# Kernel optimization log

Measured on AMD Instinct MI355X. Metric: run time of the kernel, lower is better.

The kernel has to match this reference:

```python
import jax, jax.numpy as jnp
import numpy as np

T = 2048        # flattened tokens (one prefill sequence)
HID = 2048      # hidden_size
NH = 32         # query heads
NKV = 4         # kv heads
HD = 128        # head_dim
THETA = 1000000.0
EPS = 1e-6


def setup_inputs() -> dict:
    key = jax.random.key(0)
    k0, k1, k2 = jax.random.split(key, 3)
    return {
        "positions": jnp.arange(T, dtype=jnp.int32),
        "hidden_states": jax.random.normal(k0, (T, HID), dtype=jnp.float32),
        "w_qkv": jax.random.normal(k1, ((NH + 2 * NKV) * HD, HID), dtype=jnp.float32) * 0.02,
        "w_o": jax.random.normal(k2, (HID, NH * HD), dtype=jnp.float32) * 0.02,
        "q_norm_w": jnp.ones((HD,), dtype=jnp.float32),
        "k_norm_w": jnp.ones((HD,), dtype=jnp.float32),
    }


def _rmsnorm(x, w):
    # per-head RMSNorm over last dim (head_dim), fp32 math
    var = jnp.mean(x * x, axis=-1, keepdims=True)
    return x * jax.lax.rsqrt(var + EPS) * w


def _rope(x, positions):
    # NeoX-style rotary embedding over full head_dim
    d = x.shape[-1]
    inv_freq = 1.0 / (THETA ** (jnp.arange(0, d, 2, dtype=jnp.float32) / d))  # [d/2]
    ang = positions.astype(jnp.float32)[:, None] * inv_freq                   # [T, d/2]
    cos = jnp.cos(ang)[:, None, :]  # [T,1,d/2]
    sin = jnp.sin(ang)[:, None, :]
    x1, x2 = jnp.split(x, 2, axis=-1)
    return jnp.concatenate([x1 * cos - x2 * sin, x2 * cos + x1 * sin], axis=-1)


def reference(positions, hidden_states, w_qkv, w_o, q_norm_w, k_norm_w):
    # fused QKV projection (no bias)
    qkv = hidden_states @ w_qkv.T                       # [T, (NH+2*NKV)*HD]
    q, k, v = jnp.split(qkv, [NH * HD, (NH + NKV) * HD], axis=-1)
    q = _rmsnorm(q.reshape(T, NH, HD), q_norm_w)        # [T,NH,HD]
    k = _rmsnorm(k.reshape(T, NKV, HD), k_norm_w)       # [T,NKV,HD]
    v = v.reshape(T, NKV, HD)
    q = _rope(q, positions)
    k = _rope(k, positions)
    # GQA: expand kv heads to query heads
    g = NH // NKV
    k = jnp.repeat(k, g, axis=1)                        # [T,NH,HD]
    v = jnp.repeat(v, g, axis=1)
    scale = HD ** -0.5
    scores = jnp.einsum('qhd,khd->hqk', q, k) * scale   # [NH,T,T]
    causal = jnp.tril(jnp.ones((T, T), dtype=bool))
    scores = jnp.where(causal[None, :, :], scores, jnp.finfo(scores.dtype).min)
    attn = jax.nn.softmax(scores, axis=-1)
    o = jnp.einsum('hqk,khd->qhd', attn, v).reshape(T, NH * HD)
    return o @ w_o.T                                    # [T,HID]
```

## Files before the change

### kernel.cpp

```cpp
#include <hip/hip_runtime.h>
#include <math.h>

#define T 2048
#define HID 2048
#define NH 32
#define NKV 4
#define HD 128
#define QKV_DIM 5120
#define OD 4096
#define C2LOG 0.12751743f
#define MFIX 6.0f

typedef _Float16 half8 __attribute__((ext_vector_type(8)));
typedef _Float16 half4v __attribute__((ext_vector_type(4)));
typedef float floatx4 __attribute__((ext_vector_type(4)));

#define GLD16(gp, lp) __builtin_amdgcn_global_load_lds( \
    (const __attribute__((address_space(1))) void*)(gp), \
    (__attribute__((address_space(3))) void*)(lp), 16, 0, 0)

__global__ __launch_bounds__(256)
void cvt_all(const float* __restrict__ h, const float* __restrict__ wq,
             const float* __restrict__ wo, _Float16* __restrict__ out) {
    size_t i = ((size_t)blockIdx.x * 256 + threadIdx.x) * 4;
    const float* src;
    size_t off;
    if (i < (size_t)T * HID)                        { src = h;  off = i; }
    else if (i < (size_t)T * HID + (size_t)QKV_DIM * HID)
                                                    { src = wq; off = i - (size_t)T * HID; }
    else                                            { src = wo; off = i - (size_t)T * HID - (size_t)QKV_DIM * HID; }
    float4 v = *(const float4*)(src + off);
    half4v o = { (_Float16)v.x, (_Float16)v.y, (_Float16)v.z, (_Float16)v.w };
    *(half4v*)(out + i) = o;
}

__global__ __launch_bounds__(256)
void gemm_sk_h(const _Float16* __restrict__ A, const _Float16* __restrict__ B,
               _Float16* __restrict__ p0, _Float16* __restrict__ p1,
               int M, int N, int K, int KS) {
    __shared__ __align__(16) _Float16 Asm[8192];
    __shared__ __align__(16) _Float16 Bsm[8192];
    int tid = threadIdx.x;
    int wave = tid >> 6, lane = tid & 63;
    int quad = lane >> 4, l16 = lane & 15;
    int m0 = blockIdx.y * 128, n0 = blockIdx.x * 128;
    int koff = blockIdx.z * KS;
    _Float16* C = blockIdx.z ? p1 : p0;
    int wm = (wave >> 1) * 64, wn = (wave & 1) * 64;
    const _Float16* Ag = A + (size_t)(m0 + (tid >> 2)) * K + koff + (tid & 3) * 8;
    const _Float16* Bg = B + (size_t)(n0 + (tid >> 2)) * K + koff + (tid & 3) * 8;
    size_t row64 = (size_t)64 * K;
    int wofs = wave * 512;
    floatx4 acc[4][4] = {};
    int nt = KS >> 5;
    GLD16(Ag, Asm + wofs);
    GLD16(Ag + row64, Asm + 2048 + wofs);
    GLD16(Bg, Bsm + wofs);
    GLD16(Bg + row64, Bsm + 2048 + wofs);
    for (int t = 0; t < nt; t++) {
        int cur = t & 1;
        if (t + 1 < nt) {
            const _Float16* Agp = Ag + (size_t)(t + 1) * 32;
            const _Float16* Bgp = Bg + (size_t)(t + 1) * 32;
            int nb = (cur ^ 1) * 4096 + wofs;
            GLD16(Agp, Asm + nb);
            GLD16(Agp + row64, Asm + nb + 2048);
            GLD16(Bgp, Bsm + nb);
            GLD16(Bgp + row64, Bsm + nb + 2048);
            asm volatile("s_waitcnt vmcnt(4)" ::: "memory");
        } else {
            asm volatile("s_waitcnt vmcnt(0)" ::: "memory");
        }
        __builtin_amdgcn_s_barrier();
        __builtin_amdgcn_sched_barrier(0);
        int pb = cur * 4096;
        half8 af[4], bf[4];
        #pragma unroll
        for (int i = 0; i < 4; i++)
            af[i] = *(const half8*)&Asm[pb + (wm + i * 16 + l16) * 32 + quad * 8];
        #pragma unroll
        for (int j = 0; j < 4; j++)
            bf[j] = *(const half8*)&Bsm[pb + (wn + j * 16 + l16) * 32 + quad * 8];
        #pragma unroll
        for (int i = 0; i < 4; i++)
            #pragma unroll
            for (int j = 0; j < 4; j++)
                acc[i][j] = __builtin_amdgcn_mfma_f32_16x16x32_f16(af[i], bf[j], acc[i][j], 0, 0, 0);
        __builtin_amdgcn_s_barrier();
    }
    #pragma unroll
    for (int i = 0; i < 4; i++) {
        int row = m0 + wm + i * 16 + quad * 4;
        #pragma unroll
        for (int j = 0; j < 4; j++) {
            int col = n0 + wn + j * 16 + l16;
            #pragma unroll
            for (int r = 0; r < 4; r++)
                C[(size_t)(row + r) * N + col] = (_Float16)acc[i][j][r];
        }
    }
}

__global__ __launch_bounds__(256)
void gemm_sk_f(const _Float16* __restrict__ A, const _Float16* __restrict__ B,
               _Float16* __restrict__ p0, _Float16* __restrict__ p1,
               _Float16* __restrict__ p2, _Float16* __restrict__ p3,
               int M, int N, int K, int KS) {
    __shared__ __align__(16) _Float16 Asm[8192];
    __shared__ __align__(16) _Float16 Bsm[8192];
    int tid = threadIdx.x;
    int wave = tid >> 6, lane = tid & 63;
    int quad = lane >> 4, l16 = lane & 15;
    int m0 = blockIdx.y * 128, n0 = blockIdx.x * 128;
    int bz = blockIdx.z;
    int koff = bz * KS;
    _Float16* C = (bz == 0) ? p0 : (bz == 1) ? p1 : (bz == 2) ? p2 : p3;
    int wm = (wave >> 1) * 64, wn = (wave & 1) * 64;
    const _Float16* Ag = A + (size_t)(m0 + (tid >> 2)) * K + koff + (tid & 3) * 8;
    const _Float16* Bg = B + (size_t)(n0 + (tid >> 2)) * K + koff + (tid & 3) * 8;
    size_t row64 = (size_t)64 * K;
    int wofs = wave * 512;
    floatx4 acc[4][4] = {};
    int nt = KS >> 5;
    GLD16(Ag, Asm + wofs);
    GLD16(Ag + row64, Asm + 2048 + wofs);
    GLD16(Bg, Bsm + wofs);
    GLD16(Bg + row64, Bsm + 2048 + wofs);
    for (int t = 0; t < nt; t++) {
        int cur = t & 1;
        if (t + 1 < nt) {
            const _Float16* Agp = Ag + (size_t)(t + 1) * 32;
            const _Float16* Bgp = Bg + (size_t)(t + 1) * 32;
            int nb = (cur ^ 1) * 4096 + wofs;
            GLD16(Agp, Asm + nb);
            GLD16(Agp + row64, Asm + nb + 2048);
            GLD16(Bgp, Bsm + nb);
            GLD16(Bgp + row64, Bsm + nb + 2048);
            asm volatile("s_waitcnt vmcnt(4)" ::: "memory");
        } else {
            asm volatile("s_waitcnt vmcnt(0)" ::: "memory");
        }
        __builtin_amdgcn_s_barrier();
        __builtin_amdgcn_sched_barrier(0);
        int pb = cur * 4096;
        half8 af[4], bf[4];
        #pragma unroll
        for (int i = 0; i < 4; i++)
            af[i] = *(const half8*)&Asm[pb + (wm + i * 16 + l16) * 32 + quad * 8];
        #pragma unroll
        for (int j = 0; j < 4; j++)
            bf[j] = *(const half8*)&Bsm[pb + (wn + j * 16 + l16) * 32 + quad * 8];
        #pragma unroll
        for (int i = 0; i < 4; i++)
            #pragma unroll
            for (int j = 0; j < 4; j++)
                acc[i][j] = __builtin_amdgcn_mfma_f32_16x16x32_f16(af[i], bf[j], acc[i][j], 0, 0, 0);
        __builtin_amdgcn_s_barrier();
    }
    #pragma unroll
    for (int i = 0; i < 4; i++) {
        int row = m0 + wm + i * 16 + quad * 4;
        #pragma unroll
        for (int j = 0; j < 4; j++) {
            int col = n0 + wn + j * 16 + l16;
            #pragma unroll
            for (int r = 0; r < 4; r++)
                C[(size_t)(row + r) * N + col] = (_Float16)acc[i][j][r];
        }
    }
}

__global__ __launch_bounds__(256)
void reduce4(const _Float16* __restrict__ p0, const _Float16* __restrict__ p1,
             const _Float16* __restrict__ p2, const _Float16* __restrict__ p3,
             float* __restrict__ out) {
    size_t i = ((size_t)blockIdx.x * 256 + threadIdx.x) * 4;
    half4v a = *(const half4v*)(p0 + i);
    half4v b = *(const half4v*)(p1 + i);
    half4v c = *(const half4v*)(p2 + i);
    half4v d = *(const half4v*)(p3 + i);
    float4 o = { (float)a.x + (float)b.x + (float)c.x + (float)d.x,
                 (float)a.y + (float)b.y + (float)c.y + (float)d.y,
                 (float)a.z + (float)b.z + (float)c.z + (float)d.z,
                 (float)a.w + (float)b.w + (float)c.w + (float)d.w };
    *(float4*)(out + i) = o;
}

__global__ __launch_bounds__(256)
void qkv_post(const _Float16* __restrict__ qp0, const _Float16* __restrict__ qp1,
              const int* __restrict__ positions,
              const float* __restrict__ qw, const float* __restrict__ kw,
              _Float16* __restrict__ Qb, _Float16* __restrict__ Kb,
              _Float16* __restrict__ Vt) {
    int t = blockIdx.x;
    int wave = threadIdx.x >> 6, lane = threadIdx.x & 63;
    float pos = (float)positions[t];
    float f = exp2f(-(float)lane * (19.9315685693241741f / 64.0f));
    float ang = pos * f;
    float s = sinf(ang), c = cosf(ang);
    const _Float16* r0 = qp0 + (size_t)t * QKV_DIM;
    const _Float16* r1 = qp1 + (size_t)t * QKV_DIM;
    for (int hh = wave; hh < NH + 2 * NKV; hh += 4) {
        float x1 = (float)r0[hh * HD + lane] + (float)r1[hh * HD + lane];
        float x2 = (float)r0[hh * HD + lane + 64] + (float)r1[hh * HD + lane + 64];
        if (hh < NH + NKV) {
            float ss = x1 * x1 + x2 * x2;
            for (int o = 1; o < 64; o <<= 1) ss += __shfl_xor(ss, o);
            float inv = rsqrtf(ss * (1.0f / HD) + 1e-6f);
            const float* w = (hh < NH) ? qw : kw;
            x1 = x1 * inv * w[lane];
            x2 = x2 * inv * w[lane + 64];
            float y1 = x1 * c - x2 * s;
            float y2 = x2 * c + x1 * s;
            _Float16* dst;
            if (hh < NH) dst = Qb + ((size_t)hh * T + t) * HD;
            else         dst = Kb + ((size_t)(hh - NH) * T + t) * HD;
            dst[lane]      = (_Float16)y1;
            dst[lane + 64] = (_Float16)y2;
        } else {
            int hk = hh - NH - NKV;
            Vt[((size_t)hk * HD + lane) * T + t]      = (_Float16)x1;
            Vt[((size_t)hk * HD + lane + 64) * T + t] = (_Float16)x2;
        }
    }
}

__global__ __launch_bounds__(256, 2)
void attn(const _Float16* __restrict__ Qb, const _Float16* __restrict__ Kb,
          const _Float16* __restrict__ Vt, _Float16* __restrict__ Ob) {
    __shared__ __align__(16) _Float16 Ksm[8192];
    __shared__ __align__(16) _Float16 Vsm[8192];
    __shared__ __align__(16) _Float16 Psm[4][2048];
    int b = blockIdx.x;
    int halfg = b >> 8;
    int idx = b & 255;
    int h = idx & 31;
    int qi = idx >> 5;
    int j = halfg ? qi : 15 - qi;
    int hk = h >> 3;
    int tid = threadIdx.x, wave = tid >> 6, lane = tid & 63;
    int quad = lane >> 4, l16 = lane & 15;
    int wbase = j * 128 + wave * 32;

    half8 aq[2][4];
    #pragma unroll
    for (int g = 0; g < 2; g++) {
        const _Float16* qp = Qb + ((size_t)h * T + wbase + g * 16 + l16) * HD + quad * 8;
        #pragma unroll
        for (int dk = 0; dk < 4; dk++)
            aq[g][dk] = *(const half8*)(qp + dk * 32);
    }
    floatx4 o_acc[2][8] = {};
    float lpart[2][4] = {};

    int krow = tid >> 4;
    const _Float16* Kg = Kb + ((size_t)hk * T + krow) * HD + ((tid & 15) ^ (krow & 7)) * 8;
    int vrow = tid >> 3;
    const _Float16* Vg = Vt + ((size_t)hk * HD + vrow) * T + ((tid & 7) ^ (vrow & 7)) * 8;
    _Float16* KsmW = Ksm + wave * 512;
    _Float16* VsmW = Vsm + wave * 512;
    _Float16* PsmW = Psm[wave];

    int ntiles = 2 * j + 2;
    for (int it = 0; it < ntiles; it++) {
        int kv0 = it * 64;
        __syncthreads();
        {
            const _Float16* kg = Kg + (size_t)kv0 * HD;
            const _Float16* vg = Vg + kv0;
            #pragma unroll
            for (int c = 0; c < 4; c++) {
                GLD16(kg + (size_t)c * (16 * HD), KsmW + c * 2048);
                GLD16(vg + (size_t)c * (32 * T), VsmW + c * 2048);
            }
        }
        __syncthreads();

        bool needmask = (it >= ntiles - 2);
        #pragma unroll
        for (int sn = 0; sn < 4; sn++) {
            int row = sn * 16 + l16;
            int rs = row & 7;
            floatx4 s0 = {}, s1 = {};
            #pragma unroll
            for (int dk = 0; dk < 4; dk++) {
                half8 kf = *(const half8*)&Ksm[row * 128 + ((dk * 4 + quad) ^ rs) * 8];
                s0 = __builtin_amdgcn_mfma_f32_16x16x32_f16(aq[0][dk], kf, s0, 0, 0, 0);
                s1 = __builtin_amdgcn_mfma_f32_16x16x32_f16(aq[1][dk], kf, s1, 0, 0, 0);
            }
            int kv = kv0 + sn * 16 + l16;
            int cb = sn * 2 + (l16 >> 3);
            #pragma unroll
            for (int g = 0; g < 2; g++) {
                floatx4 sv = g ? s1 : s0;
                int rqg = wbase + g * 16 + quad * 4;
                #pragma unroll
                for (int r = 0; r < 4; r++) {
                    float p = __builtin_amdgcn_exp2f(
                        __builtin_fmaf(sv[r], C2LOG, -MFIX));
                    if (needmask) p = (kv <= rqg + r) ? p : 0.0f;
                    lpart[g][r] += p;
                    int prow = g * 16 + quad * 4 + r;
                    PsmW[prow * 64 + ((cb ^ (prow & 7)) * 8 + (l16 & 7))] = (_Float16)p;
                }
            }
        }
        half8 ap[2][2];
        #pragma unroll
        for (int g = 0; g < 2; g++) {
            int pr = g * 16 + l16;
            ap[g][0] = *(const half8*)&PsmW[pr * 64 + ((quad ^ (pr & 7)) * 8)];
            ap[g][1] = *(const half8*)&PsmW[pr * 64 + (((4 + quad) ^ (pr & 7)) * 8)];
        }

        #pragma unroll
        for (int dn = 0; dn < 8; dn++) {
            int row = dn * 16 + l16;
            int rs = row & 7;
            half8 v0 = *(const half8*)&Vsm[row * 64 + ((quad ^ rs) * 8)];
            half8 v1 = *(const half8*)&Vsm[row * 64 + (((4 + quad) ^ rs) * 8)];
            o_acc[0][dn] = __builtin_amdgcn_mfma_f32_16x16x32_f16(ap[0][0], v0, o_acc[0][dn], 0, 0, 0);
            o_acc[0][dn] = __builtin_amdgcn_mfma_f32_16x16x32_f16(ap[0][1], v1, o_acc[0][dn], 0, 0, 0);
            o_acc[1][dn] = __builtin_amdgcn_mfma_f32_16x16x32_f16(ap[1][0], v0, o_acc[1][dn], 0, 0, 0);
            o_acc[1][dn] = __builtin_amdgcn_mfma_f32_16x16x32_f16(ap[1][1], v1, o_acc[1][dn], 0, 0, 0);
        }
    }

    #pragma unroll
    for (int g = 0; g < 2; g++) {
        #pragma unroll
        for (int o = 1; o < 16; o <<= 1)
            #pragma unroll
            for (int r = 0; r < 4; r++)
                lpart[g][r] += __shfl_xor(lpart[g][r], o);
        float linv[4];
        #pragma unroll
        for (int r = 0; r < 4; r++) linv[r] = 1.0f / lpart[g][r];
        int rowb = wbase + g * 16 + quad * 4;
        #pragma unroll
        for (int dn = 0; dn < 8; dn++) {
            int col = h * HD + dn * 16 + l16;
            #pragma unroll
            for (int r = 0; r < 4; r++)
                Ob[(size_t)(rowb + r) * OD + col] = (_Float16)(o_acc[g][dn][r] * linv[r]);
        }
    }
}

extern "C" void kernel_launch(void* const* d_in, const int* in_sizes, int n_in,
                              void* d_out, int out_size, void* d_ws, size_t ws_size,
                              hipStream_t stream) {
    const int*   positions = (const int*)d_in[0];
    const float* hidden    = (const float*)d_in[1];
    const float* w_qkv     = (const float*)d_in[2];
    const float* w_o       = (const float*)d_in[3];
    const float* q_norm_w  = (const float*)d_in[4];
    const float* k_norm_w  = (const float*)d_in[5];
    float* out = (float*)d_out;

    const size_t MiB = 1048576;
    char* ws = (char*)d_ws;
    _Float16* hb    = (_Float16*)(ws);
    _Float16* wqkvb = (_Float16*)(ws + 8 * MiB);
    _Float16* wob   = (_Float16*)(ws + 28 * MiB);
    _Float16* qkvp0 = (_Float16*)(ws + 44 * MiB);
    _Float16* qkvp1 = (_Float16*)(ws + 64 * MiB);
    _Float16* Qb    = (_Float16*)(ws + 84 * MiB);
    _Float16* Kb    = (_Float16*)(ws + 100 * MiB);
    _Float16* Vt    = (_Float16*)(ws + 102 * MiB);
    _Float16* Ob    = (_Float16*)(ws + 104 * MiB);
    _Float16* op0   = (_Float16*)(ws);
    _Float16* op1   = (_Float16*)(ws + 9 * MiB);
    _Float16* op2   = (_Float16*)(ws + 44 * MiB);
    _Float16* op3   = (_Float16*)(ws + 53 * MiB);

    cvt_all<<<22528, 256, 0, stream>>>(hidden, w_qkv, w_o, hb);

    gemm_sk_h<<<dim3(QKV_DIM / 128, T / 128, 2), 256, 0, stream>>>(
        hb, wqkvb, qkvp0, qkvp1, T, QKV_DIM, HID, HID / 2);

    qkv_post<<<T, 256, 0, stream>>>(qkvp0, qkvp1, positions, q_norm_w, k_norm_w, Qb, Kb, Vt);

    attn<<<512, 256, 0, stream>>>(Qb, Kb, Vt, Ob);

    gemm_sk_f<<<dim3(HID / 128, T / 128, 4), 256, 0, stream>>>(
        Ob, wob, op0, op1, op2, op3, T, HID, OD, OD / 4);
    reduce4<<<T * HID / 1024, 256, 0, stream>>>(op0, op1, op2, op3, out);
}
```

Measured before the change: 335.1 us.

## Switch attention to 32x32x16 MFMA with transposed scores and register-resident P

Rewrites the attention inner loop to use 32x32x16 MFMA tiles, computing S^T = K·Q^T so each lane owns one query row. Probabilities are packed to fp16 in registers and rearranged with v_permlane32_swap to form the A operand for the PV MFMA. This removes the per-wave LDS staging buffer for P and its store/load round trip, and cuts the row-sum shuffle reduction to a single xor. Risks include higher register pressure from 16-wide accumulators and a scattered output store pattern.

```diff
diff --git a/kernel.cpp b/kernel.cpp
--- a/kernel.cpp
+++ b/kernel.cpp
@@ -14,10 +14,20 @@
 typedef _Float16 half8 __attribute__((ext_vector_type(8)));
 typedef _Float16 half4v __attribute__((ext_vector_type(4)));
 typedef float floatx4 __attribute__((ext_vector_type(4)));
+typedef float floatx16 __attribute__((ext_vector_type(16)));
+typedef unsigned uint4v __attribute__((ext_vector_type(4)));
 
 #define GLD16(gp, lp) __builtin_amdgcn_global_load_lds( \
     (const __attribute__((address_space(1))) void*)(gp), \
     (__attribute__((address_space(3))) void*)(lp), 16, 0, 0)
+
+__device__ __forceinline__ unsigned pk_u32(float a, float b) {
+    auto h = __builtin_amdgcn_cvt_pkrtz(a, b);
+    return __builtin_bit_cast(unsigned, h);
+}
+__device__ __forceinline__ void plswap(unsigned &a, unsigned &b) {
+    asm("v_permlane32_swap_b32 %0, %1" : "+v"(a), "+v"(b));
+}
 
 __global__ __launch_bounds__(256)
 void cvt_all(const float* __restrict__ h, const float* __restrict__ wq,
@@ -230,7 +240,6 @@
           const _Float16* __restrict__ Vt, _Float16* __restrict__ Ob) {
     __shared__ __align__(16) _Float16 Ksm[8192];
     __shared__ __align__(16) _Float16 Vsm[8192];
-    __shared__ __align__(16) _Float16 Psm[4][2048];
     int b = blockIdx.x;
     int halfg = b >> 8;
     int idx = b & 255;
@@ -239,19 +248,19 @@
     int j = halfg ? qi : 15 - qi;
     int hk = h >> 3;
     int tid = threadIdx.x, wave = tid >> 6, lane = tid & 63;
-    int quad = lane >> 4, l16 = lane & 15;
-    int wbase = j * 128 + wave * 32;
-
-    half8 aq[2][4];
-    #pragma unroll
-    for (int g = 0; g < 2; g++) {
-        const _Float16* qp = Qb + ((size_t)h * T + wbase + g * 16 + l16) * HD + quad * 8;
-        #pragma unroll
-        for (int dk = 0; dk < 4; dk++)
-            aq[g][dk] = *(const half8*)(qp + dk * 32);
-    }
-    floatx4 o_acc[2][8] = {};
-    float lpart[2][4] = {};
+    int l31 = lane & 31, hi = lane >> 5;
+    int wq0 = j * 128 + wave * 32;
+    int qa = wq0 + l31;
+
+    half8 qf[8];
+    {
+        const _Float16* qp = Qb + ((size_t)h * T + qa) * HD + hi * 8;
+        #pragma unroll
+        for (int kb = 0; kb < 8; kb++)
+            qf[kb] = *(const half8*)(qp + kb * 16);
+    }
+    floatx16 o_acc[4] = {};
+    float lsum = 0.0f;
 
     int krow = tid >> 4;
     const _Float16* Kg = Kb + ((size_t)hk * T + krow) * HD + ((tid & 15) ^ (krow & 7)) * 8;
@@ -259,7 +268,6 @@
     const _Float16* Vg = Vt + ((size_t)hk * HD + vrow) * T + ((tid & 7) ^ (vrow & 7)) * 8;
     _Float16* KsmW = Ksm + wave * 512;
     _Float16* VsmW = Vsm + wave * 512;
-    _Float16* PsmW = Psm[wave];
 
     int ntiles = 2 * j + 2;
     for (int it = 0; it < ntiles; it++) {
@@ -277,72 +285,69 @@
         __syncthreads();
 
         bool needmask = (it >= ntiles - 2);
-        #pragma unroll
-        for (int sn = 0; sn < 4; sn++) {
-            int row = sn * 16 + l16;
+        half8 af[4];
+        #pragma unroll
+        for (int s = 0; s < 2; s++) {
+            int row = s * 32 + l31;
             int rs = row & 7;
-            floatx4 s0 = {}, s1 = {};
-            #pragma unroll
-            for (int dk = 0; dk < 4; dk++) {
-                half8 kf = *(const half8*)&Ksm[row * 128 + ((dk * 4 + quad) ^ rs) * 8];
-                s0 = __builtin_amdgcn_mfma_f32_16x16x32_f16(aq[0][dk], kf, s0, 0, 0, 0);
-                s1 = __builtin_amdgcn_mfma_f32_16x16x32_f16(aq[1][dk], kf, s1, 0, 0, 0);
-            }
-            int kv = kv0 + sn * 16 + l16;
-            int cb = sn * 2 + (l16 >> 3);
-            #pragma unroll
-            for (int g = 0; g < 2; g++) {
-                floatx4 sv = g ? s1 : s0;
-                int rqg = wbase + g * 16 + quad * 4;
-                #pragma unroll
-                for (int r = 0; r < 4; r++) {
-                    float p = __builtin_amdgcn_exp2f(
-                        __builtin_fmaf(sv[r], C2LOG, -MFIX));
-                    if (needmask) p = (kv <= rqg + r) ? p : 0.0f;
-                    lpart[g][r] += p;
-                    int prow = g * 16 + quad * 4 + r;
-                    PsmW[prow * 64 + ((cb ^ (prow & 7)) * 8 + (l16 & 7))] = (_Float16)p;
+            floatx16 sc = {};
+            #pragma unroll
+            for (int kb = 0; kb < 8; kb++) {
+                half8 kf = *(const half8*)&Ksm[row * 128 + (((kb * 2 + hi) ^ rs)) * 8];
+                sc = __builtin_amdgcn_mfma_f32_32x32x16_f16(kf, qf[kb], sc, 0, 0, 0);
+            }
+            float pe[16];
+            #pragma unroll
+            for (int r = 0; r < 16; r++) {
+                float p = __builtin_amdgcn_exp2f(
+                    __builtin_fmaf(sc[r], C2LOG, -MFIX));
+                if (needmask) {
+                    int kv = kv0 + s * 32 + (r & 3) + 8 * (r >> 2) + 4 * hi;
+                    p = (kv <= qa) ? p : 0.0f;
                 }
-            }
-        }
-        half8 ap[2][2];
-        #pragma unroll
-        for (int g = 0; g < 2; g++) {
-            int pr = g * 16 + l16;
-            ap[g][0] = *(const half8*)&PsmW[pr * 64 + ((quad ^ (pr & 7)) * 8)];
-            ap[g][1] = *(const half8*)&PsmW[pr * 64 + (((4 + quad) ^ (pr & 7)) * 8)];
-        }
-
-        #pragma unroll
-        for (int dn = 0; dn < 8; dn++) {
-            int row = dn * 16 + l16;
+                lsum += p;
+                pe[r] = p;
+            }
+            #pragma unroll
+            for (int c = 0; c < 2; c++) {
+                int rb = c * 8;
+                unsigned x0 = pk_u32(pe[rb + 0], pe[rb + 1]);
+                unsigned y0 = pk_u32(pe[rb + 4], pe[rb + 5]);
+                plswap(x0, y0);
+                unsigned x1 = pk_u32(pe[rb + 2], pe[rb + 3]);
+                unsigned y1 = pk_u32(pe[rb + 6], pe[rb + 7]);
+                plswap(x1, y1);
+                uint4v w = { x0, x1, y0, y1 };
+                af[s * 2 + c] = __builtin_bit_cast(half8, w);
+            }
+        }
+        #pragma unroll
+        for (int db = 0; db < 4; db++) {
+            int row = db * 32 + l31;
             int rs = row & 7;
-            half8 v0 = *(const half8*)&Vsm[row * 64 + ((quad ^ rs) * 8)];
-            half8 v1 = *(const half8*)&Vsm[row * 64 + (((4 + quad) ^ rs) * 8)];
-            o_acc[0][dn] = __builtin_amdgcn_mfma_f32_16x16x32_f16(ap[0][0], v0, o_acc[0][dn], 0, 0, 0);
-            o_acc[0][dn] = __builtin_amdgcn_mfma_f32_16x16x32_f16(ap[0][1], v1, o_acc[0][dn], 0, 0, 0);
-            o_acc[1][dn] = __builtin_amdgcn_mfma_f32_16x16x32_f16(ap[1][0], v0, o_acc[1][dn], 0, 0, 0);
-            o_acc[1][dn] = __builtin_amdgcn_mfma_f32_16x16x32_f16(ap[1][1], v1, o_acc[1][dn], 0, 0, 0);
-        }
-    }
-
+            #pragma unroll
+            for (int c = 0; c < 4; c++) {
+                half8 vf = *(const half8*)&Vsm[row * 64 + (((c * 2 + hi) ^ rs)) * 8];
+                o_acc[db] = __builtin_amdgcn_mfma_f32_32x32x16_f16(af[c], vf, o_acc[db], 0, 0, 0);
+            }
+        }
+    }
+
+    lsum += __shfl_xor(lsum, 32);
+    float linv = 1.0f / lsum;
+    float li[16];
     #pragma unroll
-    for (int g = 0; g < 2; g++) {
-        #pragma unroll
-        for (int o = 1; o < 16; o <<= 1)
-            #pragma unroll
-            for (int r = 0; r < 4; r++)
-                lpart[g][r] += __shfl_xor(lpart[g][r], o);
-        float linv[4];
-        #pragma unroll
-        for (int r = 0; r < 4; r++) linv[r] = 1.0f / lpart[g][r];
-        int rowb = wbase + g * 16 + quad * 4;
-        #pragma unroll
-        for (int dn = 0; dn < 8; dn++) {
-            int col = h * HD + dn * 16 + l16;
-            #pragma unroll
-            for (int r = 0; r < 4; r++)
-                Ob[(size_t)(rowb + r) * OD + col] = (_Float16)(o_acc[g][dn][r] * linv[r]);
+    for (int r = 0; r < 16; r++) {
+        int rq = (r & 3) + 8 * (r >> 2) + 4 * hi;
+        li[r] = __shfl(linv, rq);
+    }
+    #pragma unroll
+    for (int db = 0; db < 4; db++) {
+        int col = h * HD + db * 32 + l31;
+        #pragma unroll
+        for (int r = 0; r < 16; r++) {
+            int rq = (r & 3) + 8 * (r >> 2) + 4 * hi;
+            Ob[(size_t)(wq0 + rq) * OD + col] = (_Float16)(o_acc[db][r] * li[r]);
         }
     }
 }
```

New measurement: 341.2 us. No clear change (+1.8%).
